# Kernel tuning notes

Measured on AMD Instinct MI355X. Metric: run time of the kernel, lower is better.

Reference implementation:

```python
import jax, jax.numpy as jnp
import numpy as np

TEMPERATURE = 1.0 / 0.07  # fixed (temperature_trainable=False)
B, D = 256, 65536


def setup_inputs() -> dict:
    key = jax.random.key(0)
    kA, kB = jax.random.split(key)
    feat_A = jax.random.normal(kA, (B, D), dtype=jnp.float32)
    feat_B = jax.random.normal(kB, (B, D), dtype=jnp.float32)
    # L2-normalize (standard for contrastive features; keeps exp(logits) finite)
    feat_A = feat_A / jnp.linalg.norm(feat_A, axis=-1, keepdims=True)
    feat_B = feat_B / jnp.linalg.norm(feat_B, axis=-1, keepdims=True)
    return {"feat_A": feat_A, "feat_B": feat_B}


def reference(feat_A, feat_B):
    # logits[i, j] = <A_i, B_j> * temperature   -- [B, B]
    logits = jnp.einsum("id,jd->ij", feat_A, feat_B) * TEMPERATURE
    pos_logits = jnp.diagonal(logits)  # [B]
    # margin=0.0, dcl=False, index=None -> neg_mask is all True, so
    # log(sum_j exp(logits)) is a full-row/col logsumexp (stable form of exp->sum->log)
    neg_A2B = jax.nn.logsumexp(logits, axis=1)  # A -> B classification
    neg_B2A = jax.nn.logsumexp(logits, axis=0)  # B -> A classification
    loss_A2B = jnp.mean(neg_A2B - pos_logits)
    loss_B2A = jnp.mean(neg_B2A - pos_logits)
    return (loss_A2B + loss_B2A) * 0.5
```

## Files before the change

kernel.cpp:

```cpp
#include <hip/hip_runtime.h>
#include <hip/hip_bf16.h>


#define D_DIM 65536
#define B_DIM 256
#define LDK 72

constexpr float TEMP = 1.0f / 0.07f;

typedef short short8 __attribute__((ext_vector_type(8)));
typedef float floatx4 __attribute__((ext_vector_type(4)));

__device__ inline unsigned short f2bf(float f) {
  unsigned u = __builtin_bit_cast(unsigned, f);
  unsigned rounding = 0x7fffu + ((u >> 16) & 1u);
  return (unsigned short)((u + rounding) >> 16);
}

__device__ inline void st_bf16x4(unsigned short* dst, float4 v) {
  uint2 u;
  u.x = (unsigned)f2bf(v.x) | ((unsigned)f2bf(v.y) << 16);
  u.y = (unsigned)f2bf(v.z) | ((unsigned)f2bf(v.w) << 16);
  *(uint2*)dst = u;
}

__global__ __launch_bounds__(256, 2) void gemm_splitk(
    const float* __restrict__ A, const float* __restrict__ Bm,
    float* __restrict__ partials, int Kc) {
  const int bid = blockIdx.x;
  const int mt = (bid & 1) * 128;
  const int nt = ((bid >> 1) & 1) * 128;
  const int chunk = bid >> 2;
  const size_t k0 = (size_t)chunk * (size_t)Kc;

  __shared__ unsigned short As[128][LDK];
  __shared__ unsigned short Bs[128][LDK];

  const int t = threadIdx.x;
  const int lane = t & 63;
  const int w = t >> 6;
  const int wm = (w & 1) * 64;
  const int wn = (w >> 1) * 64;

  const int lr = t >> 4;
  const int lc = (t & 15) * 4;

  const float* Abase = A + (size_t)(mt + lr) * D_DIM + k0 + lc;
  const float* Bbase = Bm + (size_t)(nt + lr) * D_DIM + k0 + lc;

  floatx4 acc[4][4];
#pragma unroll
  for (int mb = 0; mb < 4; ++mb)
#pragma unroll
    for (int nb = 0; nb < 4; ++nb) acc[mb][nb] = (floatx4)0.f;

  float4 ra[8], rb[8];
  const int nst = Kc >> 6;

#pragma unroll
  for (int p = 0; p < 8; ++p) {
    ra[p] = *(const float4*)(Abase + (size_t)p * 16 * D_DIM);
    rb[p] = *(const float4*)(Bbase + (size_t)p * 16 * D_DIM);
  }

  for (int s = 0; s < nst; ++s) {
#pragma unroll
    for (int p = 0; p < 8; ++p) {
      st_bf16x4(&As[lr + p * 16][lc], ra[p]);
      st_bf16x4(&Bs[lr + p * 16][lc], rb[p]);
    }
    __syncthreads();

    if (s + 1 < nst) {
      const float* Ap = Abase + (size_t)(s + 1) * 64;
      const float* Bp = Bbase + (size_t)(s + 1) * 64;
#pragma unroll
      for (int p = 0; p < 8; ++p) {
        ra[p] = *(const float4*)(Ap + (size_t)p * 16 * D_DIM);
        rb[p] = *(const float4*)(Bp + (size_t)p * 16 * D_DIM);
      }
    }

#pragma unroll
    for (int ks = 0; ks < 64; ks += 32) {
      short8 af[4], bf[4];
      const int ko = ks + (lane >> 4) * 8;
#pragma unroll
      for (int mb = 0; mb < 4; ++mb)
        af[mb] = *(const short8*)&As[wm + mb * 16 + (lane & 15)][ko];
#pragma unroll
      for (int nb = 0; nb < 4; ++nb)
        bf[nb] = *(const short8*)&Bs[wn + nb * 16 + (lane & 15)][ko];
#pragma unroll
      for (int mb = 0; mb < 4; ++mb)
#pragma unroll
        for (int nb = 0; nb < 4; ++nb)
          acc[mb][nb] = __builtin_amdgcn_mfma_f32_16x16x32_bf16(
              af[mb], bf[nb], acc[mb][nb], 0, 0, 0);
    }
    __syncthreads();
  }

  float* outp = partials + (size_t)chunk * (B_DIM * B_DIM);
#pragma unroll
  for (int mb = 0; mb < 4; ++mb) {
#pragma unroll
    for (int nb = 0; nb < 4; ++nb) {
      const int gi0 = mt + wm + mb * 16 + ((lane >> 4) * 4);
      const int gj = nt + wn + nb * 16 + (lane & 15);
#pragma unroll
      for (int r = 0; r < 4; ++r)
        outp[(size_t)(gi0 + r) * B_DIM + gj] = acc[mb][nb][r];
    }
  }
}

__global__ void reduce_rows(const float* __restrict__ partials,
                            float* __restrict__ logits,
                            float* __restrict__ out, int C) {
  const int i = blockIdx.x;
  const int j = threadIdx.x;
  const float* p = partials + (size_t)i * B_DIM + j;
  float s = 0.f;
#pragma unroll 4
  for (int c = 0; c < C; ++c) s += p[(size_t)c * (B_DIM * B_DIM)];
  const float lg = s * TEMP;
  logits[i * B_DIM + j] = lg;

  __shared__ float posv;
  if (j == i) posv = lg;

  float e = expf(lg);
#pragma unroll
  for (int off = 32; off > 0; off >>= 1) e += __shfl_down(e, off);
  __shared__ float wsum[4];
  if ((j & 63) == 0) wsum[j >> 6] = e;
  __syncthreads();
  if (j == 0) {
    const float tot = wsum[0] + wsum[1] + wsum[2] + wsum[3];
    atomicAdd(out, (logf(tot) - 2.f * posv) * (0.5f / 256.f));
  }
}

__global__ void reduce_cols(const float* __restrict__ logits,
                            float* __restrict__ out) {
  const int j = blockIdx.x;
  const int i = threadIdx.x;
  float e = expf(logits[(size_t)i * B_DIM + j]);
#pragma unroll
  for (int off = 32; off > 0; off >>= 1) e += __shfl_down(e, off);
  __shared__ float wsum[4];
  if ((i & 63) == 0) wsum[i >> 6] = e;
  __syncthreads();
  if (i == 0) {
    const float tot = wsum[0] + wsum[1] + wsum[2] + wsum[3];
    atomicAdd(out, logf(tot) * (0.5f / 256.f));
  }
}

extern "C" void kernel_launch(void* const* d_in, const int* in_sizes, int n_in,
                              void* d_out, int out_size, void* d_ws, size_t ws_size,
                              hipStream_t stream) {
  (void)in_sizes; (void)n_in; (void)out_size;
  const float* A = (const float*)d_in[0];
  const float* Bm = (const float*)d_in[1];
  float* out = (float*)d_out;

  const size_t per = (size_t)B_DIM * B_DIM * sizeof(float);
  int C = 128;
  while (C > 1 && (size_t)(C + 1) * per > ws_size) C >>= 1;
  const int Kc = D_DIM / C;

  float* logits = (float*)d_ws;
  float* partials = (float*)d_ws + (size_t)B_DIM * B_DIM;

  hipMemsetAsync(d_out, 0, sizeof(float), stream);
  gemm_splitk<<<4 * C, 256, 0, stream>>>(A, Bm, partials, Kc);
  reduce_rows<<<B_DIM, B_DIM, 0, stream>>>(partials, logits, out, C);
  reduce_cols<<<B_DIM, B_DIM, 0, stream>>>(logits, out);
}
```

Baseline: 172.1 us.

## Stream fp32 fragments directly into MFMA registers and fuse row/col reductions

Replaces the LDS-staged split-K GEMM with a register-streamed version. Each wave loads its own fp32 MFMA fragments straight from global memory, converts them to bf16 in registers and double-buffers the loads. The split changes to 32 K-chunks over 16 tiles of 64x64, and the four waves' K-partials are combined through shared memory before one partial store per chunk. Row and column logsumexp are fused into a single reduce kernel, and the memset is folded into the GEMM. This removes LDS traffic, barriers and two launches, but A and B rows are now re-read by four tiles each, the loads are less coalesced, and the bf16 rounding changes to add-0x8000 truncation.

```diff
diff --git a/kernel.cpp b/kernel.cpp
--- a/kernel.cpp
+++ b/kernel.cpp
@@ -1,181 +1,167 @@
 #include <hip/hip_runtime.h>
-#include <hip/hip_bf16.h>
 
 
 #define D_DIM 65536
 #define B_DIM 256
-#define LDK 72
+#define C_CHUNKS 32
+#define KC (D_DIM / C_CHUNKS)
+#define KCW (KC / 4)
 
 constexpr float TEMP = 1.0f / 0.07f;
 
 typedef short short8 __attribute__((ext_vector_type(8)));
 typedef float floatx4 __attribute__((ext_vector_type(4)));
 
-__device__ inline unsigned short f2bf(float f) {
-  unsigned u = __builtin_bit_cast(unsigned, f);
-  unsigned rounding = 0x7fffu + ((u >> 16) & 1u);
-  return (unsigned short)((u + rounding) >> 16);
+__device__ inline unsigned fbits(float f) { return __builtin_bit_cast(unsigned, f); }
+
+__device__ inline unsigned pkbf(float lo, float hi) {
+  unsigned ul = fbits(lo) + 0x8000u;
+  unsigned uh = fbits(hi) + 0x8000u;
+  return __builtin_amdgcn_perm(uh, ul, 0x07060302);
 }
 
-__device__ inline void st_bf16x4(unsigned short* dst, float4 v) {
-  uint2 u;
-  u.x = (unsigned)f2bf(v.x) | ((unsigned)f2bf(v.y) << 16);
-  u.y = (unsigned)f2bf(v.z) | ((unsigned)f2bf(v.w) << 16);
-  *(uint2*)dst = u;
+__device__ inline short8 cvt_frag(float4 a, float4 b) {
+  union { unsigned u[4]; short8 s; } r;
+  r.u[0] = pkbf(a.x, a.y);
+  r.u[1] = pkbf(a.z, a.w);
+  r.u[2] = pkbf(b.x, b.y);
+  r.u[3] = pkbf(b.z, b.w);
+  return r.s;
 }
 
-__global__ __launch_bounds__(256, 2) void gemm_splitk(
+__global__ __launch_bounds__(256, 2) void gemm_stream(
     const float* __restrict__ A, const float* __restrict__ Bm,
-    float* __restrict__ partials, int Kc) {
+    float* __restrict__ partials, float* __restrict__ out) {
+  if (blockIdx.x == 0 && threadIdx.x == 0) *out = 0.f;
+
   const int bid = blockIdx.x;
-  const int mt = (bid & 1) * 128;
-  const int nt = ((bid >> 1) & 1) * 128;
-  const int chunk = bid >> 2;
-  const size_t k0 = (size_t)chunk * (size_t)Kc;
-
-  __shared__ unsigned short As[128][LDK];
-  __shared__ unsigned short Bs[128][LDK];
+  const int chunk = bid >> 4;
+  const int tile = bid & 15;
+  const int mt = (tile & 3) * 64;
+  const int nt = (tile >> 2) * 64;
 
   const int t = threadIdx.x;
   const int lane = t & 63;
   const int w = t >> 6;
-  const int wm = (w & 1) * 64;
-  const int wn = (w >> 1) * 64;
+  const int r16 = lane & 15;
+  const int q = lane >> 4;
 
-  const int lr = t >> 4;
-  const int lc = (t & 15) * 4;
+  const size_t kb = (size_t)chunk * KC + (size_t)w * KCW;
 
-  const float* Abase = A + (size_t)(mt + lr) * D_DIM + k0 + lc;
-  const float* Bbase = Bm + (size_t)(nt + lr) * D_DIM + k0 + lc;
+  const float* pa[4];
+  const float* pb[4];
+#pragma unroll
+  for (int f = 0; f < 4; ++f) {
+    pa[f] = A  + (size_t)(mt + f * 16 + r16) * D_DIM + kb + q * 8;
+    pb[f] = Bm + (size_t)(nt + f * 16 + r16) * D_DIM + kb + q * 8;
+  }
 
-  floatx4 acc[4][4];
+  floatx4 acc[16];
+#pragma unroll
+  for (int i = 0; i < 16; ++i) acc[i] = (floatx4)0.f;
+
+  float4 xa[8], xb[8], ya[8], yb[8];
+
+#define LOADSET(da, db, off)                                   \
+  {                                                            \
+    _Pragma("unroll") for (int f = 0; f < 4; ++f) {            \
+      da[2 * f]     = *(const float4*)(pa[f] + (off));         \
+      da[2 * f + 1] = *(const float4*)(pa[f] + (off) + 4);     \
+      db[2 * f]     = *(const float4*)(pb[f] + (off));         \
+      db[2 * f + 1] = *(const float4*)(pb[f] + (off) + 4);     \
+    }                                                          \
+  }
+
+#define COMPUTESET(da, db)                                                    \
+  {                                                                           \
+    short8 af[4], bf[4];                                                      \
+    _Pragma("unroll") for (int f = 0; f < 4; ++f) {                           \
+      af[f] = cvt_frag(da[2 * f], da[2 * f + 1]);                             \
+      bf[f] = cvt_frag(db[2 * f], db[2 * f + 1]);                             \
+    }                                                                         \
+    _Pragma("unroll") for (int mb = 0; mb < 4; ++mb)                          \
+        _Pragma("unroll") for (int nb = 0; nb < 4; ++nb)                      \
+            acc[mb * 4 + nb] = __builtin_amdgcn_mfma_f32_16x16x32_bf16(       \
+                af[mb], bf[nb], acc[mb * 4 + nb], 0, 0, 0);                   \
+  }
+
+  LOADSET(xa, xb, 0)
+#pragma unroll 1
+  for (int g = 0; g < KCW / 64; ++g) {
+    LOADSET(ya, yb, g * 64 + 32)
+    COMPUTESET(xa, xb)
+    if (g + 1 < KCW / 64) LOADSET(xa, xb, g * 64 + 64)
+    COMPUTESET(ya, yb)
+  }
+
+  __shared__ float red[4][4096];
 #pragma unroll
   for (int mb = 0; mb < 4; ++mb)
 #pragma unroll
-    for (int nb = 0; nb < 4; ++nb) acc[mb][nb] = (floatx4)0.f;
-
-  float4 ra[8], rb[8];
-  const int nst = Kc >> 6;
-
+    for (int nb = 0; nb < 4; ++nb)
 #pragma unroll
-  for (int p = 0; p < 8; ++p) {
-    ra[p] = *(const float4*)(Abase + (size_t)p * 16 * D_DIM);
-    rb[p] = *(const float4*)(Bbase + (size_t)p * 16 * D_DIM);
-  }
-
-  for (int s = 0; s < nst; ++s) {
-#pragma unroll
-    for (int p = 0; p < 8; ++p) {
-      st_bf16x4(&As[lr + p * 16][lc], ra[p]);
-      st_bf16x4(&Bs[lr + p * 16][lc], rb[p]);
-    }
-    __syncthreads();
-
-    if (s + 1 < nst) {
-      const float* Ap = Abase + (size_t)(s + 1) * 64;
-      const float* Bp = Bbase + (size_t)(s + 1) * 64;
-#pragma unroll
-      for (int p = 0; p < 8; ++p) {
-        ra[p] = *(const float4*)(Ap + (size_t)p * 16 * D_DIM);
-        rb[p] = *(const float4*)(Bp + (size_t)p * 16 * D_DIM);
-      }
-    }
-
-#pragma unroll
-    for (int ks = 0; ks < 64; ks += 32) {
-      short8 af[4], bf[4];
-      const int ko = ks + (lane >> 4) * 8;
-#pragma unroll
-      for (int mb = 0; mb < 4; ++mb)
-        af[mb] = *(const short8*)&As[wm + mb * 16 + (lane & 15)][ko];
-#pragma unroll
-      for (int nb = 0; nb < 4; ++nb)
-        bf[nb] = *(const short8*)&Bs[wn + nb * 16 + (lane & 15)][ko];
-#pragma unroll
-      for (int mb = 0; mb < 4; ++mb)
-#pragma unroll
-        for (int nb = 0; nb < 4; ++nb)
-          acc[mb][nb] = __builtin_amdgcn_mfma_f32_16x16x32_bf16(
-              af[mb], bf[nb], acc[mb][nb], 0, 0, 0);
-    }
-    __syncthreads();
-  }
+      for (int r = 0; r < 4; ++r)
+        red[w][(mb * 16 + q * 4 + r) * 64 + nb * 16 + r16] = acc[mb * 4 + nb][r];
+  __syncthreads();
 
   float* outp = partials + (size_t)chunk * (B_DIM * B_DIM);
 #pragma unroll
-  for (int mb = 0; mb < 4; ++mb) {
-#pragma unroll
-    for (int nb = 0; nb < 4; ++nb) {
-      const int gi0 = mt + wm + mb * 16 + ((lane >> 4) * 4);
-      const int gj = nt + wn + nb * 16 + (lane & 15);
-#pragma unroll
-      for (int r = 0; r < 4; ++r)
-        outp[(size_t)(gi0 + r) * B_DIM + gj] = acc[mb][nb][r];
-    }
+  for (int jj = 0; jj < 16; ++jj) {
+    const int e = jj * 256 + t;
+    const float v = red[0][e] + red[1][e] + red[2][e] + red[3][e];
+    const int row = e >> 6, col = e & 63;
+    outp[(size_t)(mt + row) * B_DIM + nt + col] = v;
   }
+#undef LOADSET
+#undef COMPUTESET
 }
 
-__global__ void reduce_rows(const float* __restrict__ partials,
-                            float* __restrict__ logits,
-                            float* __restrict__ out, int C) {
+__global__ __launch_bounds__(256, 4) void reduce_all(
+    const float* __restrict__ partials, float* __restrict__ out) {
   const int i = blockIdx.x;
   const int j = threadIdx.x;
+
+  float s = 0.f;
   const float* p = partials + (size_t)i * B_DIM + j;
-  float s = 0.f;
-#pragma unroll 4
-  for (int c = 0; c < C; ++c) s += p[(size_t)c * (B_DIM * B_DIM)];
-  const float lg = s * TEMP;
-  logits[i * B_DIM + j] = lg;
+#pragma unroll
+  for (int c = 0; c < C_CHUNKS; ++c) s += p[(size_t)c * (B_DIM * B_DIM)];
+  const float lgr = s * TEMP;
 
   __shared__ float posv;
-  if (j == i) posv = lg;
+  if (j == i) posv = lgr;
 
-  float e = expf(lg);
+  float s2 = 0.f;
+  const float* p2 = partials + (size_t)j * B_DIM + i;
 #pragma unroll
-  for (int off = 32; off > 0; off >>= 1) e += __shfl_down(e, off);
-  __shared__ float wsum[4];
-  if ((j & 63) == 0) wsum[j >> 6] = e;
+  for (int c = 0; c < C_CHUNKS; ++c) s2 += p2[(size_t)c * (B_DIM * B_DIM)];
+  const float lgc = s2 * TEMP;
+
+  float e1 = expf(lgr);
+  float e2 = expf(lgc);
+#pragma unroll
+  for (int off = 32; off > 0; off >>= 1) {
+    e1 += __shfl_down(e1, off);
+    e2 += __shfl_down(e2, off);
+  }
+  __shared__ float w1[4], w2[4];
+  if ((j & 63) == 0) { w1[j >> 6] = e1; w2[j >> 6] = e2; }
   __syncthreads();
   if (j == 0) {
-    const float tot = wsum[0] + wsum[1] + wsum[2] + wsum[3];
-    atomicAdd(out, (logf(tot) - 2.f * posv) * (0.5f / 256.f));
-  }
-}
-
-__global__ void reduce_cols(const float* __restrict__ logits,
-                            float* __restrict__ out) {
-  const int j = blockIdx.x;
-  const int i = threadIdx.x;
-  float e = expf(logits[(size_t)i * B_DIM + j]);
-#pragma unroll
-  for (int off = 32; off > 0; off >>= 1) e += __shfl_down(e, off);
-  __shared__ float wsum[4];
-  if ((i & 63) == 0) wsum[i >> 6] = e;
-  __syncthreads();
-  if (i == 0) {
-    const float tot = wsum[0] + wsum[1] + wsum[2] + wsum[3];
-    atomicAdd(out, logf(tot) * (0.5f / 256.f));
+    const float rs = w1[0] + w1[1] + w1[2] + w1[3];
+    const float cs = w2[0] + w2[1] + w2[2] + w2[3];
+    atomicAdd(out, (logf(rs) + logf(cs) - 2.f * posv) * (0.5f / 256.f));
   }
 }
 
 extern "C" void kernel_launch(void* const* d_in, const int* in_sizes, int n_in,
                               void* d_out, int out_size, void* d_ws, size_t ws_size,
                               hipStream_t stream) {
-  (void)in_sizes; (void)n_in; (void)out_size;
+  (void)in_sizes; (void)n_in; (void)out_size; (void)ws_size;
   const float* A = (const float*)d_in[0];
   const float* Bm = (const float*)d_in[1];
   float* out = (float*)d_out;
+  float* partials = (float*)d_ws;
 
-  const size_t per = (size_t)B_DIM * B_DIM * sizeof(float);
-  int C = 128;
-  while (C > 1 && (size_t)(C + 1) * per > ws_size) C >>= 1;
-  const int Kc = D_DIM / C;
-
-  float* logits = (float*)d_ws;
-  float* partials = (float*)d_ws + (size_t)B_DIM * B_DIM;
-
-  hipMemsetAsync(d_out, 0, sizeof(float), stream);
-  gemm_splitk<<<4 * C, 256, 0, stream>>>(A, Bm, partials, Kc);
-  reduce_rows<<<B_DIM, B_DIM, 0, stream>>>(partials, logits, out, C);
-  reduce_cols<<<B_DIM, B_DIM, 0, stream>>>(logits, out);
+  gemm_stream<<<16 * C_CHUNKS, 256, 0, stream>>>(A, Bm, partials, out);
+  reduce_all<<<B_DIM, B_DIM, 0, stream>>>(partials, out);
 }
```

Result: slower. 188.5 us (+9.5%).

## Double-buffer GEMM staging, cheaper bf16 pack, fuse row/col reductions into one kernel

Applied to the files above, without the earlier changes.

The GEMM now keeps two register sets and two LDS buffers, so it prefetches two k-steps ahead and drops the trailing barrier of each step. The bf16 conversion uses a single byte-permute with round-half-up instead of round-to-nearest-even, which shifts rounding slightly. The row and column reductions are merged into one kernel that accumulates column sums with atomics, and the last block to finish computes the column logsumexp. Zero-initialisation of the output, column sums and counter moves into block 0 of the GEMM, which removes the memset launch and one kernel launch, at the cost of doubled LDS and register pressure and extra atomics.

```diff
diff --git a/kernel.cpp b/kernel.cpp
--- a/kernel.cpp
+++ b/kernel.cpp
@@ -1,5 +1,4 @@
 #include <hip/hip_runtime.h>
-#include <hip/hip_bf16.h>
 
 
 #define D_DIM 65536
@@ -11,36 +10,44 @@
 typedef short short8 __attribute__((ext_vector_type(8)));
 typedef float floatx4 __attribute__((ext_vector_type(4)));
 
-__device__ inline unsigned short f2bf(float f) {
-  unsigned u = __builtin_bit_cast(unsigned, f);
-  unsigned rounding = 0x7fffu + ((u >> 16) & 1u);
-  return (unsigned short)((u + rounding) >> 16);
+__device__ inline unsigned fbits(float f) { return __builtin_bit_cast(unsigned, f); }
+
+__device__ inline unsigned pkbf(float lo, float hi) {
+  return __builtin_amdgcn_perm(fbits(hi) + 0x8000u, fbits(lo) + 0x8000u, 0x07060302);
 }
 
 __device__ inline void st_bf16x4(unsigned short* dst, float4 v) {
   uint2 u;
-  u.x = (unsigned)f2bf(v.x) | ((unsigned)f2bf(v.y) << 16);
-  u.y = (unsigned)f2bf(v.z) | ((unsigned)f2bf(v.w) << 16);
+  u.x = pkbf(v.x, v.y);
+  u.y = pkbf(v.z, v.w);
   *(uint2*)dst = u;
 }
 
 __global__ __launch_bounds__(256, 2) void gemm_splitk(
     const float* __restrict__ A, const float* __restrict__ Bm,
-    float* __restrict__ partials, int Kc) {
+    float* __restrict__ partials, float* __restrict__ colsum,
+    float* __restrict__ out, unsigned* __restrict__ counter, int Kc) {
   const int bid = blockIdx.x;
+  const int t = threadIdx.x;
+  if (bid == 0) {
+    colsum[t] = 0.f;
+    if (t == 0) { *out = 0.f; *counter = 0u; }
+  }
+
   const int mt = (bid & 1) * 128;
   const int nt = ((bid >> 1) & 1) * 128;
   const int chunk = bid >> 2;
   const size_t k0 = (size_t)chunk * (size_t)Kc;
 
-  __shared__ unsigned short As[128][LDK];
-  __shared__ unsigned short Bs[128][LDK];
+  __shared__ unsigned short As[2][128][LDK];
+  __shared__ unsigned short Bs[2][128][LDK];
 
-  const int t = threadIdx.x;
   const int lane = t & 63;
   const int w = t >> 6;
   const int wm = (w & 1) * 64;
   const int wn = (w >> 1) * 64;
+  const int lane15 = lane & 15;
+  const int laneq = lane >> 4;
 
   const int lr = t >> 4;
   const int lc = (t & 15) * 4;
@@ -54,60 +61,63 @@
 #pragma unroll
     for (int nb = 0; nb < 4; ++nb) acc[mb][nb] = (floatx4)0.f;
 
-  float4 ra[8], rb[8];
+  float4 ra0[8], rb0[8], ra1[8], rb1[8];
   const int nst = Kc >> 6;
 
 #pragma unroll
   for (int p = 0; p < 8; ++p) {
-    ra[p] = *(const float4*)(Abase + (size_t)p * 16 * D_DIM);
-    rb[p] = *(const float4*)(Bbase + (size_t)p * 16 * D_DIM);
+    ra0[p] = *(const float4*)(Abase + (size_t)p * 16 * D_DIM);
+    rb0[p] = *(const float4*)(Bbase + (size_t)p * 16 * D_DIM);
+  }
+#pragma unroll
+  for (int p = 0; p < 8; ++p) {
+    ra1[p] = *(const float4*)(Abase + (size_t)p * 16 * D_DIM + 64);
+    rb1[p] = *(const float4*)(Bbase + (size_t)p * 16 * D_DIM + 64);
   }
 
-  for (int s = 0; s < nst; ++s) {
-#pragma unroll
-    for (int p = 0; p < 8; ++p) {
-      st_bf16x4(&As[lr + p * 16][lc], ra[p]);
-      st_bf16x4(&Bs[lr + p * 16][lc], rb[p]);
-    }
-    __syncthreads();
+#define STAGE(RA, RB, BUF, S)                                                  \
+  {                                                                            \
+    _Pragma("unroll") for (int p = 0; p < 8; ++p) {                            \
+      st_bf16x4(&As[BUF][lr + p * 16][lc], RA[p]);                             \
+      st_bf16x4(&Bs[BUF][lr + p * 16][lc], RB[p]);                             \
+    }                                                                          \
+    __syncthreads(); \
+    if ((S) + 2 < nst) {                                                       \
+      const float* Ap = Abase + (size_t)((S) + 2) * 64;                        \
+      const float* Bp = Bbase + (size_t)((S) + 2) * 64;                        \
+      _Pragma("unroll") for (int p = 0; p < 8; ++p) {                          \
+        RA[p] = *(const float4*)(Ap + (size_t)p * 16 * D_DIM);                 \
+        RB[p] = *(const float4*)(Bp + (size_t)p * 16 * D_DIM);                 \
+      }                                                                        \
+    }                                                                          \
+    _Pragma("unroll") for (int ks = 0; ks < 64; ks += 32) {                    \
+      const int ko = ks + laneq * 8;                                           \
+      short8 af[4], bf[4];                                                     \
+      _Pragma("unroll") for (int mb = 0; mb < 4; ++mb)                         \
+          af[mb] = *(const short8*)&As[BUF][wm + mb * 16 + lane15][ko];        \
+      _Pragma("unroll") for (int nb = 0; nb < 4; ++nb)                         \
+          bf[nb] = *(const short8*)&Bs[BUF][wn + nb * 16 + lane15][ko];        \
+      _Pragma("unroll") for (int mb = 0; mb < 4; ++mb)                         \
+          _Pragma("unroll") for (int nb = 0; nb < 4; ++nb)                     \
+              acc[mb][nb] = __builtin_amdgcn_mfma_f32_16x16x32_bf16(           \
+                  af[mb], bf[nb], acc[mb][nb], 0, 0, 0);                       \
+    }                                                                          \
+  }
 
-    if (s + 1 < nst) {
-      const float* Ap = Abase + (size_t)(s + 1) * 64;
-      const float* Bp = Bbase + (size_t)(s + 1) * 64;
-#pragma unroll
-      for (int p = 0; p < 8; ++p) {
-        ra[p] = *(const float4*)(Ap + (size_t)p * 16 * D_DIM);
-        rb[p] = *(const float4*)(Bp + (size_t)p * 16 * D_DIM);
-      }
-    }
-
-#pragma unroll
-    for (int ks = 0; ks < 64; ks += 32) {
-      short8 af[4], bf[4];
-      const int ko = ks + (lane >> 4) * 8;
-#pragma unroll
-      for (int mb = 0; mb < 4; ++mb)
-        af[mb] = *(const short8*)&As[wm + mb * 16 + (lane & 15)][ko];
-#pragma unroll
-      for (int nb = 0; nb < 4; ++nb)
-        bf[nb] = *(const short8*)&Bs[wn + nb * 16 + (lane & 15)][ko];
-#pragma unroll
-      for (int mb = 0; mb < 4; ++mb)
-#pragma unroll
-        for (int nb = 0; nb < 4; ++nb)
-          acc[mb][nb] = __builtin_amdgcn_mfma_f32_16x16x32_bf16(
-              af[mb], bf[nb], acc[mb][nb], 0, 0, 0);
-    }
-    __syncthreads();
+#pragma unroll 1
+  for (int s = 0; s < nst; s += 2) {
+    STAGE(ra0, rb0, 0, s)
+    STAGE(ra1, rb1, 1, s + 1)
   }
+#undef STAGE
 
   float* outp = partials + (size_t)chunk * (B_DIM * B_DIM);
 #pragma unroll
   for (int mb = 0; mb < 4; ++mb) {
+    const int gi0 = mt + wm + mb * 16 + laneq * 4;
 #pragma unroll
     for (int nb = 0; nb < 4; ++nb) {
-      const int gi0 = mt + wm + mb * 16 + ((lane >> 4) * 4);
-      const int gj = nt + wn + nb * 16 + (lane & 15);
+      const int gj = nt + wn + nb * 16 + lane15;
 #pragma unroll
       for (int r = 0; r < 4; ++r)
         outp[(size_t)(gi0 + r) * B_DIM + gj] = acc[mb][nb][r];
@@ -115,46 +125,49 @@
   }
 }
 
-__global__ void reduce_rows(const float* __restrict__ partials,
-                            float* __restrict__ logits,
-                            float* __restrict__ out, int C) {
+__global__ __launch_bounds__(256, 2) void reduce_all(
+    const float* __restrict__ partials, float* __restrict__ colsum,
+    float* __restrict__ out, unsigned* __restrict__ counter, int C) {
   const int i = blockIdx.x;
   const int j = threadIdx.x;
+
+  float s = 0.f;
   const float* p = partials + (size_t)i * B_DIM + j;
-  float s = 0.f;
-#pragma unroll 4
+#pragma unroll 8
   for (int c = 0; c < C; ++c) s += p[(size_t)c * (B_DIM * B_DIM)];
   const float lg = s * TEMP;
-  logits[i * B_DIM + j] = lg;
 
   __shared__ float posv;
   if (j == i) posv = lg;
 
-  float e = expf(lg);
+  const float e = expf(lg);
+  atomicAdd(&colsum[j], e);
+
+  float r = e;
 #pragma unroll
-  for (int off = 32; off > 0; off >>= 1) e += __shfl_down(e, off);
+  for (int off = 32; off > 0; off >>= 1) r += __shfl_down(r, off);
   __shared__ float wsum[4];
-  if ((j & 63) == 0) wsum[j >> 6] = e;
+  if ((j & 63) == 0) wsum[j >> 6] = r;
+  __threadfence();
   __syncthreads();
+
+  __shared__ bool last;
   if (j == 0) {
-    const float tot = wsum[0] + wsum[1] + wsum[2] + wsum[3];
-    atomicAdd(out, (logf(tot) - 2.f * posv) * (0.5f / 256.f));
+    const float rowsum = wsum[0] + wsum[1] + wsum[2] + wsum[3];
+    atomicAdd(out, (logf(rowsum) - 2.f * posv) * (0.5f / 256.f));
+    last = (atomicAdd(counter, 1u) == B_DIM - 1);
   }
-}
+  __syncthreads();
 
-__global__ void reduce_cols(const float* __restrict__ logits,
-                            float* __restrict__ out) {
-  const int j = blockIdx.x;
-  const int i = threadIdx.x;
-  float e = expf(logits[(size_t)i * B_DIM + j]);
+  if (last) {
+    __threadfence();
+    float cl = logf(colsum[j]);
 #pragma unroll
-  for (int off = 32; off > 0; off >>= 1) e += __shfl_down(e, off);
-  __shared__ float wsum[4];
-  if ((i & 63) == 0) wsum[i >> 6] = e;
-  __syncthreads();
-  if (i == 0) {
-    const float tot = wsum[0] + wsum[1] + wsum[2] + wsum[3];
-    atomicAdd(out, logf(tot) * (0.5f / 256.f));
+    for (int off = 32; off > 0; off >>= 1) cl += __shfl_down(cl, off);
+    if ((j & 63) == 0) wsum[j >> 6] = cl;
+    __syncthreads();
+    if (j == 0)
+      atomicAdd(out, (wsum[0] + wsum[1] + wsum[2] + wsum[3]) * (0.5f / 256.f));
   }
 }
 
@@ -168,14 +181,13 @@
 
   const size_t per = (size_t)B_DIM * B_DIM * sizeof(float);
   int C = 128;
-  while (C > 1 && (size_t)(C + 1) * per > ws_size) C >>= 1;
+  while (C > 4 && (size_t)C * per + 2048 > ws_size) C >>= 1;
   const int Kc = D_DIM / C;
 
-  float* logits = (float*)d_ws;
-  float* partials = (float*)d_ws + (size_t)B_DIM * B_DIM;
+  float* partials = (float*)d_ws;
+  float* colsum = partials + (size_t)C * B_DIM * B_DIM;
+  unsigned* counter = (unsigned*)(colsum + B_DIM);
 
-  hipMemsetAsync(d_out, 0, sizeof(float), stream);
-  gemm_splitk<<<4 * C, 256, 0, stream>>>(A, Bm, partials, Kc);
-  reduce_rows<<<B_DIM, B_DIM, 0, stream>>>(partials, logits, out, C);
-  reduce_cols<<<B_DIM, B_DIM, 0, stream>>>(logits, out);
+  gemm_splitk<<<4 * C, 256, 0, stream>>>(A, Bm, partials, colsum, out, counter, Kc);
+  reduce_all<<<B_DIM, B_DIM, 0, stream>>>(partials, colsum, out, counter, C);
 }
```

Result: slower. 176.9 us (+2.8%).
